# Optimization experiments

Measured on AMD Instinct MI355X. Metric: run time of the kernel, lower is better.

Reference implementation:

```python
import jax, jax.numpy as jnp
import numpy as np

D_MODEL = 1024
N_HEADS = 16
D_K = D_MODEL // N_HEADS
B, S = 4, 2048


def setup_inputs() -> dict:
    key = jax.random.key(0)
    ks = jax.random.split(key, 5)
    scale = 1.0 / np.sqrt(D_MODEL)  # ~xavier scale for square matrices
    return {
        "Q": jax.random.normal(ks[0], (B, S, D_MODEL), dtype=jnp.float32),
        "length": jax.random.randint(ks[1], (B,), 1, S, dtype=jnp.int32),
        "Wq": jax.random.normal(ks[2], (D_MODEL, D_MODEL), dtype=jnp.float32) * scale,
        "bq": jnp.zeros((D_MODEL,), dtype=jnp.float32),
        "Wk": jax.random.normal(ks[3], (D_MODEL, D_MODEL), dtype=jnp.float32) * scale,
        "bk": jnp.zeros((D_MODEL,), dtype=jnp.float32),
        "Wv": jax.random.normal(ks[4], (D_MODEL, D_MODEL), dtype=jnp.float32) * scale,
        "bv": jnp.zeros((D_MODEL,), dtype=jnp.float32),
    }


def reference(Q, length, Wq, bq, Wk, bk, Wv, bv):
    b, s, d = Q.shape
    q_a = Q @ Wq + bq                                   # [b, s, d]
    # split heads: [b, h, s, d_k]
    q_s = q_a.reshape(b, s, N_HEADS, D_K).transpose(0, 2, 1, 3)
    k_s = (Q @ Wk + bk).reshape(b, s, N_HEADS, D_K).transpose(0, 2, 1, 3)
    v_s = (Q @ Wv + bv).reshape(b, s, N_HEADS, D_K).transpose(0, 2, 1, 3)

    # unnormalized exp attention with multiplicative key mask (faithful to source)
    scores = jnp.einsum("bhqd,bhkd->bhqk", q_s, k_s) / np.sqrt(D_K)
    scores = jnp.exp(scores)
    key_mask = (jnp.arange(s)[None, :] < length[:, None]).astype(scores.dtype)  # [b, k]
    scores = scores * key_mask[:, None, None, :]        # broadcast over heads, queries
    attn = scores / (jnp.sum(scores, axis=-1, keepdims=True) + 1e-8)
    context = jnp.einsum("bhqk,bhkd->bhqd", attn, v_s)
    context = context.transpose(0, 2, 1, 3).reshape(b, s, d)
    return context, q_a
```

## Files before the change

### kernel.cpp

```cpp
#include <hip/hip_runtime.h>

#define D_MODEL 1024
#define N_HEADS 16
#define D_KH    64
#define BATCH   4
#define SEQ     2048
#define M_TOTAL (BATCH*SEQ)

typedef __attribute__((ext_vector_type(8))) short short8;
typedef __attribute__((ext_vector_type(4))) float f32x4;
typedef __attribute__((ext_vector_type(4))) unsigned short u16x4;
typedef __attribute__((ext_vector_type(2))) unsigned int u32x2;

__device__ __forceinline__ unsigned short f2bf(float f) {
  union { float f; unsigned u; } v; v.f = f;
  unsigned r = v.u + 0x7FFFu + ((v.u >> 16) & 1u);
  return (unsigned short)(r >> 16);
}
__device__ __forceinline__ unsigned fbits(float f) {
  union { float f; unsigned u; } v; v.f = f; return v.u;
}

__global__ __launch_bounds__(256) void cvt_q(const float* __restrict__ Q,
                                             unsigned short* __restrict__ Qbf) {
  size_t i = (size_t)blockIdx.x * 256 + threadIdx.x;
  float4 v = ((const float4*)Q)[i];
  u16x4 o;
  o[0] = f2bf(v.x); o[1] = f2bf(v.y); o[2] = f2bf(v.z); o[3] = f2bf(v.w);
  ((u16x4*)Qbf)[i] = o;
}

__global__ __launch_bounds__(256) void cvt_wt(const float* __restrict__ Wq,
                                              const float* __restrict__ Wk,
                                              const float* __restrict__ Wv,
                                              unsigned short* __restrict__ WT) {
  const int z = blockIdx.z;
  const float* W = (z == 0) ? Wq : (z == 1) ? Wk : Wv;
  __shared__ float tile[32][33];
  const int k0 = blockIdx.y * 32, n0 = blockIdx.x * 32;
  const int tx = threadIdx.x & 31, ty = threadIdx.x >> 5;
  for (int i = 0; i < 4; ++i)
    tile[ty + i * 8][tx] = W[(size_t)(k0 + ty + i * 8) * D_MODEL + n0 + tx];
  __syncthreads();
  unsigned short* out = WT + (size_t)z * D_MODEL * D_MODEL;
  for (int i = 0; i < 4; ++i)
    out[(size_t)(n0 + ty + i * 8) * D_MODEL + k0 + tx] = f2bf(tile[tx][ty + i * 8]);
}

#define BM 128
#define BN 128
#define BK 32

__global__ __launch_bounds__(256, 2) void gemm_qkv(
    const unsigned short* __restrict__ Qbf,
    const unsigned short* __restrict__ WT,
    const float* __restrict__ bq_p, const float* __restrict__ bk_p,
    const float* __restrict__ bv_p,
    float* __restrict__ out_qa,
    unsigned short* __restrict__ kbf,
    unsigned short* __restrict__ vt) {
  const int z  = blockIdx.z;
  const int n0 = blockIdx.x * BN;
  const int m0 = blockIdx.y * BM;
  const int K  = D_MODEL;

  __shared__ unsigned short smA[BM * BK];
  __shared__ unsigned short smB[BN * BK];

  const int t    = threadIdx.x;
  const int lane = t & 63;
  const int w    = t >> 6;
  const int quad = lane >> 4;
  const int l16  = lane & 15;
  const int wr   = w >> 1, wc = w & 1;

  const unsigned short* Wz = WT + (size_t)z * D_MODEL * D_MODEL;

  f32x4 acc[4][4];
  for (int i = 0; i < 4; ++i)
    for (int j = 0; j < 4; ++j) acc[i][j] = (f32x4){0.f, 0.f, 0.f, 0.f};

  for (int k0 = 0; k0 < K; k0 += BK) {
    __syncthreads();
    for (int it = 0; it < 2; ++it) {
      int c   = t + it * 256;
      int row = c >> 2, col = (c & 3) * 8;
      const unsigned short* ga = Qbf + (size_t)(m0 + row) * K + k0 + col;
      const unsigned short* gb = Wz  + (size_t)(n0 + row) * K + k0 + col;
      __builtin_amdgcn_global_load_lds(
          (const __attribute__((address_space(1))) void*)ga,
          (__attribute__((address_space(3))) void*)&smA[c * 8], 16, 0, 0);
      __builtin_amdgcn_global_load_lds(
          (const __attribute__((address_space(1))) void*)gb,
          (__attribute__((address_space(3))) void*)&smB[c * 8], 16, 0, 0);
    }
    __syncthreads();

    short8 afr[4], bfr[4];
    for (int mi = 0; mi < 4; ++mi)
      afr[mi] = *(const short8*)&smA[(wr * 64 + mi * 16 + l16) * BK + quad * 8];
    for (int ni = 0; ni < 4; ++ni)
      bfr[ni] = *(const short8*)&smB[(wc * 64 + ni * 16 + l16) * BK + quad * 8];
    for (int mi = 0; mi < 4; ++mi)
      for (int ni = 0; ni < 4; ++ni)
        acc[mi][ni] = __builtin_amdgcn_mfma_f32_16x16x32_bf16(
            afr[mi], bfr[ni], acc[mi][ni], 0, 0, 0);
  }

  const float* bias = (z == 0) ? bq_p : (z == 1) ? bk_p : bv_p;
  if (z == 2) {
    for (int ni = 0; ni < 4; ++ni) {
      int n = n0 + wc * 64 + ni * 16 + l16;
      float bval = bias[n];
      int h = n >> 6, d = n & 63;
      for (int mi = 0; mi < 4; ++mi) {
        int m = m0 + wr * 64 + mi * 16 + quad * 4;
        int b = m >> 11, s = m & 2047;
        u16x4 o;
        for (int j = 0; j < 4; ++j) o[j] = f2bf(acc[mi][ni][j] + bval);
        *(u16x4*)&vt[(size_t)((b * 16 + h) * 64 + d) * SEQ + s] = o;
      }
    }
  } else {
    for (int ni = 0; ni < 4; ++ni) {
      int n = n0 + wc * 64 + ni * 16 + l16;
      float bval = bias[n];
      for (int mi = 0; mi < 4; ++mi) {
        int mbase = m0 + wr * 64 + mi * 16 + quad * 4;
        for (int j = 0; j < 4; ++j) {
          float v = acc[mi][ni][j] + bval;
          size_t idx = (size_t)(mbase + j) * D_MODEL + n;
          if (z == 0) out_qa[idx] = v;
          else        kbf[idx] = f2bf(v);
        }
      }
    }
  }
}

#define PST 72

__global__ __launch_bounds__(256, 4) void attn(
    const float* __restrict__ qa,
    const unsigned short* __restrict__ kbf,
    const unsigned short* __restrict__ vt,
    const int* __restrict__ length,
    float* __restrict__ ctx) {
  const int qt = blockIdx.x;
  const int bh = blockIdx.y;
  const int b = bh >> 4, h = bh & 15;
  const int len = length[b];

  const int t    = threadIdx.x;
  const int lane = t & 63;
  const int w    = t >> 6;
  const int quad = lane >> 4;
  const int l16  = lane & 15;
  const int r8   = t >> 3;
  const int c8   = (t & 7) * 8;

  __shared__ unsigned short sQ[64 * PST];
  __shared__ unsigned short sK[64 * PST];
  __shared__ unsigned short sVT[64 * PST];
  __shared__ unsigned short sP[64 * PST];

  const float SCL = 0.125f * 1.44269504f;

  for (int half = 0; half < 2; ++half) {
    int r = r8 + half * 32;
    const float* src = qa + (size_t)(b * SEQ + qt * 64 + r) * D_MODEL + h * D_KH + c8;
    float4 v0 = *(const float4*)src;
    float4 v1 = *(const float4*)(src + 4);
    short8 o;
    o[0] = (short)f2bf(v0.x * SCL); o[1] = (short)f2bf(v0.y * SCL);
    o[2] = (short)f2bf(v0.z * SCL); o[3] = (short)f2bf(v0.w * SCL);
    o[4] = (short)f2bf(v1.x * SCL); o[5] = (short)f2bf(v1.y * SCL);
    o[6] = (short)f2bf(v1.z * SCL); o[7] = (short)f2bf(v1.w * SCL);
    *(short8*)&sQ[r * PST + c8] = o;
  }
  __syncthreads();

  short8 qf0 = *(const short8*)&sQ[(w * 16 + l16) * PST + quad * 8];
  short8 qf1 = *(const short8*)&sQ[(w * 16 + l16) * PST + 32 + quad * 8];

  f32x4 accpv[4];
  for (int i = 0; i < 4; ++i) accpv[i] = (f32x4){0.f, 0.f, 0.f, 0.f};
  float den = 0.f;

  const unsigned short* kbase_p = kbf + (size_t)b * SEQ * D_MODEL + h * D_KH;
  const unsigned short* vbase_p = vt + (size_t)bh * 64 * SEQ;

  const int nkt = (len + 63) >> 6;

  short8 rk[2], rv[2];
  for (int half = 0; half < 2; ++half) {
    int r = r8 + half * 32;
    rk[half] = *(const short8*)(kbase_p + (size_t)r * D_MODEL + c8);
    rv[half] = *(const short8*)(vbase_p + (size_t)r * SEQ + c8);
  }

  for (int kt = 0; kt < nkt; ++kt) {
    __syncthreads();
    for (int half = 0; half < 2; ++half) {
      int r = r8 + half * 32;
      *(short8*)&sK[r * PST + c8]  = rk[half];
      *(short8*)&sVT[r * PST + c8] = rv[half];
    }
    __syncthreads();

    if (kt + 1 < nkt) {
      for (int half = 0; half < 2; ++half) {
        int r = r8 + half * 32;
        rk[half] = *(const short8*)(kbase_p + (size_t)((kt + 1) * 64 + r) * D_MODEL + c8);
        rv[half] = *(const short8*)(vbase_p + (size_t)r * SEQ + (kt + 1) * 64 + c8);
      }
    }

    const bool full = ((kt + 1) << 6) <= len;

    for (int n = 0; n < 4; ++n) {
      short8 kf0 = *(const short8*)&sK[(n * 16 + l16) * PST + quad * 8];
      short8 kf1 = *(const short8*)&sK[(n * 16 + l16) * PST + 32 + quad * 8];
      f32x4 s = (f32x4){0.f, 0.f, 0.f, 0.f};
      s = __builtin_amdgcn_mfma_f32_16x16x32_bf16(kf0, qf0, s, 0, 0, 0);
      s = __builtin_amdgcn_mfma_f32_16x16x32_bf16(kf1, qf1, s, 0, 0, 0);
      float e0, e1, e2, e3;
      if (full) {
        e0 = exp2f(s[0]); e1 = exp2f(s[1]);
        e2 = exp2f(s[2]); e3 = exp2f(s[3]);
      } else {
        int kb = kt * 64 + n * 16 + quad * 4;
        e0 = (kb + 0 < len) ? exp2f(s[0]) : 0.f;
        e1 = (kb + 1 < len) ? exp2f(s[1]) : 0.f;
        e2 = (kb + 2 < len) ? exp2f(s[2]) : 0.f;
        e3 = (kb + 3 < len) ? exp2f(s[3]) : 0.f;
      }
      den += (e0 + e1) + (e2 + e3);
      u32x2 pk;
      pk[0] = __builtin_amdgcn_perm(fbits(e1), fbits(e0), 0x07060302);
      pk[1] = __builtin_amdgcn_perm(fbits(e3), fbits(e2), 0x07060302);
      *(u32x2*)&sP[(w * 16 + l16) * PST + n * 16 + quad * 4] = pk;
    }

    short8 pf0 = *(const short8*)&sP[(w * 16 + l16) * PST + quad * 8];
    short8 pf1 = *(const short8*)&sP[(w * 16 + l16) * PST + 32 + quad * 8];
    for (int n2 = 0; n2 < 4; ++n2) {
      short8 vf0 = *(const short8*)&sVT[(n2 * 16 + l16) * PST + quad * 8];
      short8 vf1 = *(const short8*)&sVT[(n2 * 16 + l16) * PST + 32 + quad * 8];
      accpv[n2] = __builtin_amdgcn_mfma_f32_16x16x32_bf16(vf0, pf0, accpv[n2], 0, 0, 0);
      accpv[n2] = __builtin_amdgcn_mfma_f32_16x16x32_bf16(vf1, pf1, accpv[n2], 0, 0, 0);
    }
  }

  den += __shfl_xor(den, 16, 64);
  den += __shfl_xor(den, 32, 64);
  float inv = 1.f / (den + 1e-8f);

  {
    int q = qt * 64 + w * 16 + l16;
    float* dst = ctx + (size_t)(b * SEQ + q) * D_MODEL + h * D_KH;
    for (int n2 = 0; n2 < 4; ++n2) {
      f32x4 o = accpv[n2];
      float4 v = make_float4(o[0] * inv, o[1] * inv, o[2] * inv, o[3] * inv);
      *(float4*)(dst + n2 * 16 + quad * 4) = v;
    }
  }
}

extern "C" void kernel_launch(void* const* d_in, const int* in_sizes, int n_in,
                              void* d_out, int out_size, void* d_ws, size_t ws_size,
                              hipStream_t stream) {
  const float* Q      = (const float*)d_in[0];
  const int*   length = (const int*)d_in[1];
  const float* Wq     = (const float*)d_in[2];
  const float* bq     = (const float*)d_in[3];
  const float* Wk     = (const float*)d_in[4];
  const float* bk     = (const float*)d_in[5];
  const float* Wv     = (const float*)d_in[6];
  const float* bv     = (const float*)d_in[7];

  float* out_ctx = (float*)d_out;
  float* out_qa  = out_ctx + (size_t)M_TOTAL * D_MODEL;

  char* ws = (char*)d_ws;
  unsigned short* Qbf = (unsigned short*)ws;
  unsigned short* WT  = (unsigned short*)(ws + (size_t)16 * 1024 * 1024);
  unsigned short* Kbf = (unsigned short*)(ws + (size_t)22 * 1024 * 1024);
  unsigned short* Vt  = (unsigned short*)(ws + (size_t)38 * 1024 * 1024);

  hipLaunchKernelGGL(cvt_q, dim3((M_TOTAL * D_MODEL) / (256 * 4)), dim3(256), 0, stream,
                     Q, Qbf);
  hipLaunchKernelGGL(cvt_wt, dim3(32, 32, 3), dim3(256), 0, stream, Wq, Wk, Wv, WT);
  hipLaunchKernelGGL(gemm_qkv, dim3(D_MODEL / BN, M_TOTAL / BM, 3), dim3(256), 0, stream,
                     Qbf, WT, bq, bk, bv, out_qa, Kbf, Vt);
  hipLaunchKernelGGL(attn, dim3(SEQ / 64, BATCH * N_HEADS), dim3(256), 0, stream,
                     out_qa, Kbf, Vt, length, out_ctx);
}
```

Baseline: 255.4 us.

## Widen attention query tile to 128 rows and interleave batches across blocks

The attention kernel now processes 128 query rows per block with 512 threads. Each 64-key K/V tile staged in shared memory is therefore reused by eight waves instead of four, halving K/V global traffic per query. The probability buffer is aliased onto the Q staging buffer to save LDS. Block indices are remapped so that neighbouring blocks get different batches, which spreads the variable-length key loops more evenly across CUs. The launch bound of (512, 8) may push the compiler into tight register limits or spills, and fewer, larger blocks leave less scheduling slack.

```diff
diff --git a/kernel.cpp b/kernel.cpp
--- a/kernel.cpp
+++ b/kernel.cpp
@@ -139,16 +139,22 @@
 }
 
 #define PST 72
-
-__global__ __launch_bounds__(256, 4) void attn(
+#define QBLK 128
+
+__global__ __launch_bounds__(512, 8) void attn(
     const float* __restrict__ qa,
     const unsigned short* __restrict__ kbf,
     const unsigned short* __restrict__ vt,
     const int* __restrict__ length,
     float* __restrict__ ctx) {
-  const int qt = blockIdx.x;
-  const int bh = blockIdx.y;
-  const int b = bh >> 4, h = bh & 15;
+  const int flat = blockIdx.y * 16 + blockIdx.x;
+  const int low = flat & 3;
+  const int mid = (flat >> 2) & 15;
+  const int hi  = flat >> 6;
+  const int b  = (low + mid + (mid >> 2) + hi + (hi >> 2)) & 3;
+  const int h  = mid;
+  const int qt = hi;
+  const int bh = b * 16 + h;
   const int len = length[b];
 
   const int t    = threadIdx.x;
@@ -159,16 +165,16 @@
   const int r8   = t >> 3;
   const int c8   = (t & 7) * 8;
 
-  __shared__ unsigned short sQ[64 * PST];
+  __shared__ unsigned short sQ[QBLK * PST];
   __shared__ unsigned short sK[64 * PST];
   __shared__ unsigned short sVT[64 * PST];
-  __shared__ unsigned short sP[64 * PST];
+  unsigned short* const sP = sQ;
 
   const float SCL = 0.125f * 1.44269504f;
 
   for (int half = 0; half < 2; ++half) {
-    int r = r8 + half * 32;
-    const float* src = qa + (size_t)(b * SEQ + qt * 64 + r) * D_MODEL + h * D_KH + c8;
+    int r = r8 + half * 64;
+    const float* src = qa + (size_t)(b * SEQ + qt * QBLK + r) * D_MODEL + h * D_KH + c8;
     float4 v0 = *(const float4*)src;
     float4 v1 = *(const float4*)(src + 4);
     short8 o;
@@ -192,28 +198,18 @@
 
   const int nkt = (len + 63) >> 6;
 
-  short8 rk[2], rv[2];
-  for (int half = 0; half < 2; ++half) {
-    int r = r8 + half * 32;
-    rk[half] = *(const short8*)(kbase_p + (size_t)r * D_MODEL + c8);
-    rv[half] = *(const short8*)(vbase_p + (size_t)r * SEQ + c8);
-  }
+  short8 rk = *(const short8*)(kbase_p + (size_t)r8 * D_MODEL + c8);
+  short8 rv = *(const short8*)(vbase_p + (size_t)r8 * SEQ + c8);
 
   for (int kt = 0; kt < nkt; ++kt) {
     __syncthreads();
-    for (int half = 0; half < 2; ++half) {
-      int r = r8 + half * 32;
-      *(short8*)&sK[r * PST + c8]  = rk[half];
-      *(short8*)&sVT[r * PST + c8] = rv[half];
-    }
+    *(short8*)&sK[r8 * PST + c8]  = rk;
+    *(short8*)&sVT[r8 * PST + c8] = rv;
     __syncthreads();
 
     if (kt + 1 < nkt) {
-      for (int half = 0; half < 2; ++half) {
-        int r = r8 + half * 32;
-        rk[half] = *(const short8*)(kbase_p + (size_t)((kt + 1) * 64 + r) * D_MODEL + c8);
-        rv[half] = *(const short8*)(vbase_p + (size_t)r * SEQ + (kt + 1) * 64 + c8);
-      }
+      rk = *(const short8*)(kbase_p + (size_t)((kt + 1) * 64 + r8) * D_MODEL + c8);
+      rv = *(const short8*)(vbase_p + (size_t)r8 * SEQ + (kt + 1) * 64 + c8);
     }
 
     const bool full = ((kt + 1) << 6) <= len;
@@ -257,7 +253,7 @@
   float inv = 1.f / (den + 1e-8f);
 
   {
-    int q = qt * 64 + w * 16 + l16;
+    int q = qt * QBLK + w * 16 + l16;
     float* dst = ctx + (size_t)(b * SEQ + q) * D_MODEL + h * D_KH;
     for (int n2 = 0; n2 < 4; ++n2) {
       f32x4 o = accpv[n2];
@@ -293,6 +289,6 @@
   hipLaunchKernelGGL(cvt_wt, dim3(32, 32, 3), dim3(256), 0, stream, Wq, Wk, Wv, WT);
   hipLaunchKernelGGL(gemm_qkv, dim3(D_MODEL / BN, M_TOTAL / BM, 3), dim3(256), 0, stream,
                      Qbf, WT, bq, bk, bv, out_qa, Kbf, Vt);
-  hipLaunchKernelGGL(attn, dim3(SEQ / 64, BATCH * N_HEADS), dim3(256), 0, stream,
+  hipLaunchKernelGGL(attn, dim3(SEQ / QBLK, BATCH * N_HEADS), dim3(512), 0, stream,
                      out_qa, Kbf, Vt, length, out_ctx);
 }
```

Measured after the change: 274.7 us. +7.6%, slower.

## Process 128 queries per attention block and remap blocks to balance batch lengths

Applied to the files above, without the earlier changes.

Each attention workgroup now handles 128 query rows instead of 64, with every wave computing two 16-row query tiles against each loaded K/V tile. This halves the global K/V traffic and the shared-memory staging per query. The P buffer now reuses the Q shared array, since Q fragments are held in registers after the initial load. The grid shrinks to 1024 blocks, and a flat-index remap interleaves batches so blocks with different sequence lengths spread across CUs. The cost is more registers per thread and fewer blocks to hide latency.

```diff
diff --git a/kernel.cpp b/kernel.cpp
--- a/kernel.cpp
+++ b/kernel.cpp
@@ -139,6 +139,7 @@
 }
 
 #define PST 72
+#define QBLK 128
 
 __global__ __launch_bounds__(256, 4) void attn(
     const float* __restrict__ qa,
@@ -146,9 +147,14 @@
     const unsigned short* __restrict__ vt,
     const int* __restrict__ length,
     float* __restrict__ ctx) {
-  const int qt = blockIdx.x;
-  const int bh = blockIdx.y;
-  const int b = bh >> 4, h = bh & 15;
+  const int flat = blockIdx.y * 16 + blockIdx.x;
+  const int low = flat & 3;
+  const int mid = (flat >> 2) & 15;
+  const int hi  = flat >> 6;
+  const int b  = (low + mid + (mid >> 2) + hi + (hi >> 2)) & 3;
+  const int h  = mid;
+  const int qt = hi;
+  const int bh = b * 16 + h;
   const int len = length[b];
 
   const int t    = threadIdx.x;
@@ -159,16 +165,16 @@
   const int r8   = t >> 3;
   const int c8   = (t & 7) * 8;
 
-  __shared__ unsigned short sQ[64 * PST];
+  __shared__ unsigned short sQ[QBLK * PST];
   __shared__ unsigned short sK[64 * PST];
   __shared__ unsigned short sVT[64 * PST];
-  __shared__ unsigned short sP[64 * PST];
+  unsigned short* const sP = sQ;
 
   const float SCL = 0.125f * 1.44269504f;
 
-  for (int half = 0; half < 2; ++half) {
+  for (int half = 0; half < 4; ++half) {
     int r = r8 + half * 32;
-    const float* src = qa + (size_t)(b * SEQ + qt * 64 + r) * D_MODEL + h * D_KH + c8;
+    const float* src = qa + (size_t)(b * SEQ + qt * QBLK + r) * D_MODEL + h * D_KH + c8;
     float4 v0 = *(const float4*)src;
     float4 v1 = *(const float4*)(src + 4);
     short8 o;
@@ -180,12 +186,17 @@
   }
   __syncthreads();
 
-  short8 qf0 = *(const short8*)&sQ[(w * 16 + l16) * PST + quad * 8];
-  short8 qf1 = *(const short8*)&sQ[(w * 16 + l16) * PST + 32 + quad * 8];
-
-  f32x4 accpv[4];
-  for (int i = 0; i < 4; ++i) accpv[i] = (f32x4){0.f, 0.f, 0.f, 0.f};
-  float den = 0.f;
+  short8 qf00 = *(const short8*)&sQ[(w * 16 + l16) * PST + quad * 8];
+  short8 qf01 = *(const short8*)&sQ[(w * 16 + l16) * PST + 32 + quad * 8];
+  short8 qf10 = *(const short8*)&sQ[(64 + w * 16 + l16) * PST + quad * 8];
+  short8 qf11 = *(const short8*)&sQ[(64 + w * 16 + l16) * PST + 32 + quad * 8];
+
+  f32x4 acc0[4], acc1[4];
+  for (int i = 0; i < 4; ++i) {
+    acc0[i] = (f32x4){0.f, 0.f, 0.f, 0.f};
+    acc1[i] = (f32x4){0.f, 0.f, 0.f, 0.f};
+  }
+  float den0 = 0.f, den1 = 0.f;
 
   const unsigned short* kbase_p = kbf + (size_t)b * SEQ * D_MODEL + h * D_KH;
   const unsigned short* vbase_p = vt + (size_t)bh * 64 * SEQ;
@@ -221,48 +232,72 @@
     for (int n = 0; n < 4; ++n) {
       short8 kf0 = *(const short8*)&sK[(n * 16 + l16) * PST + quad * 8];
       short8 kf1 = *(const short8*)&sK[(n * 16 + l16) * PST + 32 + quad * 8];
-      f32x4 s = (f32x4){0.f, 0.f, 0.f, 0.f};
-      s = __builtin_amdgcn_mfma_f32_16x16x32_bf16(kf0, qf0, s, 0, 0, 0);
-      s = __builtin_amdgcn_mfma_f32_16x16x32_bf16(kf1, qf1, s, 0, 0, 0);
-      float e0, e1, e2, e3;
+      f32x4 s0 = (f32x4){0.f, 0.f, 0.f, 0.f};
+      s0 = __builtin_amdgcn_mfma_f32_16x16x32_bf16(kf0, qf00, s0, 0, 0, 0);
+      s0 = __builtin_amdgcn_mfma_f32_16x16x32_bf16(kf1, qf01, s0, 0, 0, 0);
+      f32x4 s1 = (f32x4){0.f, 0.f, 0.f, 0.f};
+      s1 = __builtin_amdgcn_mfma_f32_16x16x32_bf16(kf0, qf10, s1, 0, 0, 0);
+      s1 = __builtin_amdgcn_mfma_f32_16x16x32_bf16(kf1, qf11, s1, 0, 0, 0);
+
+      float e0, e1, e2, e3, f0, f1, f2, f3;
       if (full) {
-        e0 = exp2f(s[0]); e1 = exp2f(s[1]);
-        e2 = exp2f(s[2]); e3 = exp2f(s[3]);
+        e0 = exp2f(s0[0]); e1 = exp2f(s0[1]); e2 = exp2f(s0[2]); e3 = exp2f(s0[3]);
+        f0 = exp2f(s1[0]); f1 = exp2f(s1[1]); f2 = exp2f(s1[2]); f3 = exp2f(s1[3]);
       } else {
         int kb = kt * 64 + n * 16 + quad * 4;
-        e0 = (kb + 0 < len) ? exp2f(s[0]) : 0.f;
-        e1 = (kb + 1 < len) ? exp2f(s[1]) : 0.f;
-        e2 = (kb + 2 < len) ? exp2f(s[2]) : 0.f;
-        e3 = (kb + 3 < len) ? exp2f(s[3]) : 0.f;
+        e0 = (kb + 0 < len) ? exp2f(s0[0]) : 0.f;
+        e1 = (kb + 1 < len) ? exp2f(s0[1]) : 0.f;
+        e2 = (kb + 2 < len) ? exp2f(s0[2]) : 0.f;
+        e3 = (kb + 3 < len) ? exp2f(s0[3]) : 0.f;
+        f0 = (kb + 0 < len) ? exp2f(s1[0]) : 0.f;
+        f1 = (kb + 1 < len) ? exp2f(s1[1]) : 0.f;
+        f2 = (kb + 2 < len) ? exp2f(s1[2]) : 0.f;
+        f3 = (kb + 3 < len) ? exp2f(s1[3]) : 0.f;
       }
-      den += (e0 + e1) + (e2 + e3);
+      den0 += (e0 + e1) + (e2 + e3);
+      den1 += (f0 + f1) + (f2 + f3);
       u32x2 pk;
       pk[0] = __builtin_amdgcn_perm(fbits(e1), fbits(e0), 0x07060302);
       pk[1] = __builtin_amdgcn_perm(fbits(e3), fbits(e2), 0x07060302);
       *(u32x2*)&sP[(w * 16 + l16) * PST + n * 16 + quad * 4] = pk;
-    }
-
-    short8 pf0 = *(const short8*)&sP[(w * 16 + l16) * PST + quad * 8];
-    short8 pf1 = *(const short8*)&sP[(w * 16 + l16) * PST + 32 + quad * 8];
+      u32x2 pk1;
+      pk1[0] = __builtin_amdgcn_perm(fbits(f1), fbits(f0), 0x07060302);
+      pk1[1] = __builtin_amdgcn_perm(fbits(f3), fbits(f2), 0x07060302);
+      *(u32x2*)&sP[(64 + w * 16 + l16) * PST + n * 16 + quad * 4] = pk1;
+    }
+
+    short8 pf00 = *(const short8*)&sP[(w * 16 + l16) * PST + quad * 8];
+    short8 pf01 = *(const short8*)&sP[(w * 16 + l16) * PST + 32 + quad * 8];
+    short8 pf10 = *(const short8*)&sP[(64 + w * 16 + l16) * PST + quad * 8];
+    short8 pf11 = *(const short8*)&sP[(64 + w * 16 + l16) * PST + 32 + quad * 8];
     for (int n2 = 0; n2 < 4; ++n2) {
       short8 vf0 = *(const short8*)&sVT[(n2 * 16 + l16) * PST + quad * 8];
       short8 vf1 = *(const short8*)&sVT[(n2 * 16 + l16) * PST + 32 + quad * 8];
-      accpv[n2] = __builtin_amdgcn_mfma_f32_16x16x32_bf16(vf0, pf0, accpv[n2], 0, 0, 0);
-      accpv[n2] = __builtin_amdgcn_mfma_f32_16x16x32_bf16(vf1, pf1, accpv[n2], 0, 0, 0);
-    }
-  }
-
-  den += __shfl_xor(den, 16, 64);
-  den += __shfl_xor(den, 32, 64);
-  float inv = 1.f / (den + 1e-8f);
+      acc0[n2] = __builtin_amdgcn_mfma_f32_16x16x32_bf16(vf0, pf00, acc0[n2], 0, 0, 0);
+      acc0[n2] = __builtin_amdgcn_mfma_f32_16x16x32_bf16(vf1, pf01, acc0[n2], 0, 0, 0);
+      acc1[n2] = __builtin_amdgcn_mfma_f32_16x16x32_bf16(vf0, pf10, acc1[n2], 0, 0, 0);
+      acc1[n2] = __builtin_amdgcn_mfma_f32_16x16x32_bf16(vf1, pf11, acc1[n2], 0, 0, 0);
+    }
+  }
+
+  den0 += __shfl_xor(den0, 16, 64);
+  den0 += __shfl_xor(den0, 32, 64);
+  den1 += __shfl_xor(den1, 16, 64);
+  den1 += __shfl_xor(den1, 32, 64);
+  float inv0 = 1.f / (den0 + 1e-8f);
+  float inv1 = 1.f / (den1 + 1e-8f);
 
   {
-    int q = qt * 64 + w * 16 + l16;
-    float* dst = ctx + (size_t)(b * SEQ + q) * D_MODEL + h * D_KH;
+    int q0 = qt * QBLK + w * 16 + l16;
+    float* dst0 = ctx + (size_t)(b * SEQ + q0) * D_MODEL + h * D_KH;
+    float* dst1 = dst0 + (size_t)64 * D_MODEL;
     for (int n2 = 0; n2 < 4; ++n2) {
-      f32x4 o = accpv[n2];
-      float4 v = make_float4(o[0] * inv, o[1] * inv, o[2] * inv, o[3] * inv);
-      *(float4*)(dst + n2 * 16 + quad * 4) = v;
+      f32x4 o0 = acc0[n2];
+      f32x4 o1 = acc1[n2];
+      *(float4*)(dst0 + n2 * 16 + quad * 4) =
+          make_float4(o0[0] * inv0, o0[1] * inv0, o0[2] * inv0, o0[3] * inv0);
+      *(float4*)(dst1 + n2 * 16 + quad * 4) =
+          make_float4(o1[0] * inv1, o1[1] * inv1, o1[2] * inv1, o1[3] * inv1);
     }
   }
 }
@@ -293,6 +328,6 @@
   hipLaunchKernelGGL(cvt_wt, dim3(32, 32, 3), dim3(256), 0, stream, Wq, Wk, Wv, WT);
   hipLaunchKernelGGL(gemm_qkv, dim3(D_MODEL / BN, M_TOTAL / BM, 3), dim3(256), 0, stream,
                      Qbf, WT, bq, bk, bv, out_qa, Kbf, Vt);
-  hipLaunchKernelGGL(attn, dim3(SEQ / 64, BATCH * N_HEADS), dim3(256), 0, stream,
+  hipLaunchKernelGGL(attn, dim3(SEQ / QBLK, BATCH * N_HEADS), dim3(256), 0, stream,
                      out_qa, Kbf, Vt, length, out_ctx);
 }
```

New measurement: 255.8 us. No clear change (+0.2%).
